# Kernel optimization log

Hardware: AMD Instinct MI355X
Metric: run time of the kernel (lower is better)

The kernel has to match this reference:

```python
import jax, jax.numpy as jnp
import numpy as np

B, CIN, COUT, K, H, W = 8, 256, 256, 3, 64, 64
STRIDE, PAD, DIL, DG = 1, 1, 1, 1
K2 = K * K


def _conv2d(x, w, b):
    out = jax.lax.conv_general_dilated(
        x, w, (STRIDE, STRIDE), [(PAD, PAD), (PAD, PAD)],
        rhs_dilation=(DIL, DIL),
        dimension_numbers=('NCHW', 'OIHW', 'NCHW'))
    return out + b[None, :, None, None]


def _deform_conv2d(x, offset, mask, weight, bias):
    # torchvision.ops.deform_conv2d semantics (DCNv2, bilinear, zero outside).
    Bn, Cin, Hin, Win = x.shape
    O = weight.shape[0]
    dg, Cg = DG, Cin // DG
    Ho, Wo = offset.shape[2], offset.shape[3]
    # offset channel layout: [dg, K2, (dy,dx)] interleaved per kernel point
    off = offset.reshape(Bn, dg, K2, 2, Ho, Wo)
    dy, dx = off[:, :, :, 0], off[:, :, :, 1]
    m = mask.reshape(Bn, dg, K2, Ho, Wo)
    ky, kx = jnp.meshgrid(jnp.arange(K), jnp.arange(K), indexing='ij')
    ky = ky.reshape(K2).astype(x.dtype)
    kx = kx.reshape(K2).astype(x.dtype)
    base_y = jnp.arange(Ho, dtype=x.dtype) * STRIDE - PAD
    base_x = jnp.arange(Wo, dtype=x.dtype) * STRIDE - PAD
    # sampling positions [B, dg, K2, Ho, Wo]
    py = base_y[None, None, None, :, None] + (ky * DIL)[None, None, :, None, None] + dy
    px = base_x[None, None, None, None, :] + (kx * DIL)[None, None, :, None, None] + dx
    y0 = jnp.floor(py)
    x0 = jnp.floor(px)
    ly, lx = py - y0, px - x0

    xflat = x.reshape(Bn, dg, Cg, Hin * Win)

    def gather_one(xg, idx):
        return jnp.take(xg, idx, axis=1)

    gather = jax.vmap(jax.vmap(gather_one))  # over B, dg

    def corner(yc, xc, wgt):
        valid = (yc >= 0) & (yc <= Hin - 1) & (xc >= 0) & (xc <= Win - 1)
        yi = jnp.clip(yc, 0, Hin - 1).astype(jnp.int32)
        xi = jnp.clip(xc, 0, Win - 1).astype(jnp.int32)
        idx = (yi * Win + xi).reshape(Bn, dg, K2 * Ho * Wo)
        v = gather(xflat, idx).reshape(Bn, dg, Cg, K2, Ho, Wo)
        w = jnp.where(valid, wgt, jnp.zeros_like(wgt))
        return v * w[:, :, None]  # broadcast over Cg

    sampled = (corner(y0, x0, (1 - ly) * (1 - lx))
               + corner(y0, x0 + 1, (1 - ly) * lx)
               + corner(y0 + 1, x0, ly * (1 - lx))
               + corner(y0 + 1, x0 + 1, ly * lx))
    sampled = sampled * m[:, :, None]  # modulation mask
    wk = weight.reshape(O, dg, Cg, K2)
    out = jnp.einsum('ogck,bgckhw->bohw', wk, sampled)
    return out + bias[None, :, None, None]


def reference(x, weight, bias, w_off, b_off):
    om = _conv2d(x, w_off, b_off)  # [B, 3*dg*K2, H, W]
    n = DG * K2
    o1, o2, mask = om[:, :n], om[:, n:2 * n], om[:, 2 * n:]
    offset = jnp.concatenate([o1, o2], axis=1)
    mask = jax.nn.sigmoid(mask)
    return _deform_conv2d(x, offset, mask, weight, bias)


def setup_inputs():
    key = jax.random.key(0)
    k1, k2, k3, k4, k5 = jax.random.split(key, 5)
    fan_in = CIN * K2
    bound = 1.0 / np.sqrt(fan_in).astype(np.float32)
    x = jax.random.normal(k1, (B, CIN, H, W), dtype=jnp.float32)
    weight = jax.random.uniform(k2, (COUT, CIN, K, K), minval=-bound, maxval=bound, dtype=jnp.float32)
    bias = jax.random.uniform(k3, (COUT,), minval=-bound, maxval=bound, dtype=jnp.float32)
    # small random offset-conv params (zero init in the source is degenerate)
    w_off = jax.random.normal(k4, (3 * K2 * DG, CIN, K, K), dtype=jnp.float32) * 0.01
    b_off = jax.random.normal(k5, (3 * K2 * DG,), dtype=jnp.float32) * 0.01
    return {"x": x, "weight": weight, "bias": bias, "w_off": w_off, "b_off": b_off}
```

## Files before the change

### kernel.cpp

```cpp
#include <hip/hip_runtime.h>
#include <hip/hip_bf16.h>
#include <stdint.h>

typedef short bf16x8 __attribute__((ext_vector_type(8)));
typedef float f32x4  __attribute__((ext_vector_type(4)));

#define NB   8
#define NC   256
#define NO   256
#define HH   64
#define WW   64
#define NPIX 4096
#define KTOT 2304
#define NKC  72

#define XN_OFF  0u
#define XN_SZ   (NB*NPIX*NC*2u)
#define WP_OFF  (XN_OFF + XN_SZ)
#define WP_SZ   (KTOT*NO*2u)
#define WPO_OFF (WP_OFF + WP_SZ)
#define WPO_SZ  (KTOT*32u*2u)
#define OM_OFF  (WPO_OFF + WPO_SZ)
#define OM_SZ   (NB*NPIX*32u*4u)
#define PY_OFF  (OM_OFF + OM_SZ)
#define CO_SZ   (NB*9u*NPIX*4u)
#define PX_OFF  (PY_OFF + CO_SZ)
#define MK_OFF  (PX_OFF + CO_SZ)

__device__ __forceinline__ float b2f(short s) {
    union { unsigned u; float f; } z; z.u = ((unsigned)(unsigned short)s) << 16; return z.f;
}
__device__ __forceinline__ short f2b(float f) {
    __hip_bfloat16 h = __float2bfloat16(f);
    short s; __builtin_memcpy(&s, &h, 2); return s;
}

__global__ void pack_x(const float* __restrict__ x, unsigned short* __restrict__ xn) {
    __shared__ float tile[64][65];
    int blk = blockIdx.x;
    int pt = blk & 63, ct = (blk >> 6) & 3, b = blk >> 8;
    int t = threadIdx.x;
    int pi = t & 63, ci0 = t >> 6;
    const float* src = x + ((size_t)(b*NC + ct*64))*NPIX + (size_t)pt*64;
#pragma unroll
    for (int j = 0; j < 16; ++j)
        tile[ci0 + 4*j][pi] = src[(size_t)(ci0 + 4*j)*NPIX + pi];
    __syncthreads();
    int c = t & 63, pj0 = t >> 6;
    unsigned short* dst = xn + ((size_t)b*NPIX + (size_t)pt*64)*NC + ct*64;
#pragma unroll
    for (int j = 0; j < 16; ++j) {
        int pj = pj0 + 4*j;
        dst[(size_t)pj*NC + c] = (unsigned short)f2b(tile[c][pj]);
    }
}

__global__ void pack_w(const float* __restrict__ weight, unsigned short* __restrict__ wp) {
    int idx = blockIdx.x*256 + threadIdx.x;
    int e = idx & 7, l = (idx >> 3) & 63, nt = (idx >> 9) & 15, kc = idx >> 13;
    int k  = kc*32 + 8*(l >> 4) + e;
    int k2 = k >> 8, c = k & 255;
    int ky = k2 / 3, kx = k2 - 3*ky;
    int o  = nt*16 + (l & 15);
    float v = weight[(size_t)(o*NC + c)*9 + ky*3 + kx];
    wp[idx] = (unsigned short)f2b(v);
}

__global__ void pack_wo(const float* __restrict__ w_off, unsigned short* __restrict__ wpo) {
    int idx = blockIdx.x*256 + threadIdx.x;
    int e = idx & 7, l = (idx >> 3) & 63, nt = (idx >> 9) & 1, kc = idx >> 10;
    int k  = kc*32 + 8*(l >> 4) + e;
    int k2 = k >> 8, c = k & 255;
    int ky = k2 / 3, kx = k2 - 3*ky;
    int n  = nt*16 + (l & 15);
    float v = (n < 27) ? w_off[(size_t)(n*NC + c)*9 + ky*3 + kx] : 0.0f;
    wpo[idx] = (unsigned short)f2b(v);
}

__launch_bounds__(256, 2)
__global__ void off_conv(const unsigned short* __restrict__ xn,
                         const unsigned short* __restrict__ wpo,
                         float* __restrict__ om) {
    int blk = blockIdx.x;
    int mt = blk & 63, b = blk >> 6;
    int t = threadIdx.x, wv = t >> 6, l = t & 63, g = l >> 4;
    int pix = mt*64 + wv*16 + (l & 15);
    int y = pix >> 6, xx = pix & 63;
    f32x4 acc0 = {0.f,0.f,0.f,0.f}, acc1 = {0.f,0.f,0.f,0.f};
    const unsigned short* xb = xn + (size_t)b*NPIX*NC;
    const bf16x8* wpf = (const bf16x8*)wpo;
    for (int kc = 0; kc < NKC; ++kc) {
        int k2 = kc >> 3, cc = kc & 7;
        int ky = k2 / 3, kx = k2 - 3*ky;
        int sy = y + ky - 1, sx = xx + kx - 1;
        bool valid = (sy >= 0) & (sy < HH) & (sx >= 0) & (sx < WW);
        bf16x8 a = {0,0,0,0,0,0,0,0};
        if (valid)
            a = *(const bf16x8*)(xb + (size_t)(sy*WW + sx)*NC + cc*32 + g*8);
        bf16x8 b0 = wpf[(size_t)(kc*2    )*64 + l];
        bf16x8 b1 = wpf[(size_t)(kc*2 + 1)*64 + l];
        acc0 = __builtin_amdgcn_mfma_f32_16x16x32_bf16(a, b0, acc0, 0, 0, 0);
        acc1 = __builtin_amdgcn_mfma_f32_16x16x32_bf16(a, b1, acc1, 0, 0, 0);
    }
#pragma unroll
    for (int r = 0; r < 4; ++r) {
        int pm = mt*64 + wv*16 + 4*g + r;
        om[((size_t)b*NPIX + pm)*32 +      (l & 15)] = acc0[r];
        om[((size_t)b*NPIX + pm)*32 + 16 + (l & 15)] = acc1[r];
    }
}

__global__ void coords_k(const float* __restrict__ om, const float* __restrict__ b_off,
                         float* __restrict__ py, float* __restrict__ px,
                         float* __restrict__ mk) {
    int idx = blockIdx.x*256 + threadIdx.x;
    if (idx >= NB*9*NPIX) return;
    int pix = idx & 4095;
    int k   = (idx >> 12) % 9;
    int b   = idx / (9*NPIX);
    const float* omp = om + ((size_t)b*NPIX + pix)*32;
    float dy = omp[2*k]     + b_off[2*k];
    float dx = omp[2*k + 1] + b_off[2*k + 1];
    float m  = omp[18 + k]  + b_off[18 + k];
    float yy = (float)(pix >> 6) - 1.0f + (float)(k / 3) + dy;
    float xv = (float)(pix & 63) - 1.0f + (float)(k % 3) + dx;
    py[idx] = yy;
    px[idx] = xv;
    mk[idx] = 1.0f / (1.0f + __expf(-m));
}

__launch_bounds__(256, 2)
__global__ void dcn_main(const unsigned short* __restrict__ xn,
                         const unsigned short* __restrict__ wpack,
                         const float* __restrict__ pyA,
                         const float* __restrict__ pxA,
                         const float* __restrict__ mkA,
                         const float* __restrict__ bias,
                         float* __restrict__ out) {
    __shared__ unsigned short lds[2][8192];
    int blk = blockIdx.x;
    int mt = blk & 63, b = blk >> 6;
    int t = threadIdx.x, wv = t >> 6, l = t & 63, g = l >> 4;
    int pixm = mt*64 + wv*16 + (l & 15);

    f32x4 acc[16];
#pragma unroll
    for (int i = 0; i < 16; ++i) acc[i] = f32x4{0.f,0.f,0.f,0.f};

    const unsigned short* xb = xn + (size_t)b*NPIX*NC;

#define STAGE(bi, kcs) do {                                                            \
        const unsigned short* _gs = wpack + (size_t)(kcs)*8192 + wv*2048 + l*8;        \
        _Pragma("unroll")                                                              \
        for (int _i = 0; _i < 4; ++_i) {                                               \
            __builtin_amdgcn_global_load_lds(                                          \
                (const __attribute__((address_space(1))) unsigned int*)(_gs + _i*512), \
                (__attribute__((address_space(3))) unsigned int*)(&lds[bi][wv*2048 + _i*512]), \
                16, 0, 0);                                                             \
        }                                                                              \
    } while (0)

    float cw0 = 0.f, cw1 = 0.f, cw2 = 0.f, cw3 = 0.f;
    unsigned ca0 = 0, ca1 = 0, ca2 = 0, ca3 = 0;

    STAGE(0, 0);
    __syncthreads();
    int buf = 0;
    for (int kc = 0; kc < NKC; ++kc) {
        int k2 = kc >> 3, cc = kc & 7;
        if (cc == 0) {
            int ci = ((b*9 + k2) << 12) + pixm;
            float py = pyA[ci], px = pxA[ci], m = mkA[ci];
            float y0f = floorf(py), x0f = floorf(px);
            float ly = py - y0f, lx = px - x0f;
            int iy0 = (int)y0f, ix0 = (int)x0f;
            int iy1 = iy0 + 1,  ix1 = ix0 + 1;
            bool vy0 = (iy0 >= 0) & (iy0 < HH);
            bool vy1 = (iy1 >= 0) & (iy1 < HH);
            bool vx0 = (ix0 >= 0) & (ix0 < WW);
            bool vx1 = (ix1 >= 0) & (ix1 < WW);
            float wy0 = (1.f - ly) * m, wy1 = ly * m;
            cw0 = (vy0 & vx0) ? wy0 * (1.f - lx) : 0.f;
            cw1 = (vy0 & vx1) ? wy0 * lx         : 0.f;
            cw2 = (vy1 & vx0) ? wy1 * (1.f - lx) : 0.f;
            cw3 = (vy1 & vx1) ? wy1 * lx         : 0.f;
            int cy0 = min(max(iy0, 0), HH-1), cy1 = min(max(iy1, 0), HH-1);
            int cx0 = min(max(ix0, 0), WW-1), cx1 = min(max(ix1, 0), WW-1);
            ca0 = (unsigned)(((cy0*WW + cx0)*NC + g*8) * 2);
            ca1 = (unsigned)(((cy0*WW + cx1)*NC + g*8) * 2);
            ca2 = (unsigned)(((cy1*WW + cx0)*NC + g*8) * 2);
            ca3 = (unsigned)(((cy1*WW + cx1)*NC + g*8) * 2);
        }
        if (kc < NKC-1) STAGE(buf ^ 1, kc + 1);

        unsigned co = (unsigned)cc * 64u;
        const char* xc = (const char*)xb;
        bf16x8 v00 = *(const bf16x8*)(xc + ca0 + co);
        bf16x8 v01 = *(const bf16x8*)(xc + ca1 + co);
        bf16x8 v10 = *(const bf16x8*)(xc + ca2 + co);
        bf16x8 v11 = *(const bf16x8*)(xc + ca3 + co);
        bf16x8 a;
#pragma unroll
        for (int e = 0; e < 8; ++e) {
            float f = cw0*b2f(v00[e]) + cw1*b2f(v01[e]) + cw2*b2f(v10[e]) + cw3*b2f(v11[e]);
            a[e] = f2b(f);
        }
        const bf16x8* bl = (const bf16x8*)&lds[buf][0];
#pragma unroll
        for (int nt = 0; nt < 16; ++nt)
            acc[nt] = __builtin_amdgcn_mfma_f32_16x16x32_bf16(a, bl[nt*64 + l], acc[nt], 0, 0, 0);
        __syncthreads();
        buf ^= 1;
    }
#undef STAGE

    int pm = mt*64 + wv*16 + 4*g;
#pragma unroll
    for (int nt = 0; nt < 16; ++nt) {
        int o = nt*16 + (l & 15);
        float bv = bias[o];
        f32x4 r = acc[nt] + bv;
        *(f32x4*)(out + ((size_t)(b*NO + o))*NPIX + pm) = r;
    }
}

extern "C" void kernel_launch(void* const* d_in, const int* in_sizes, int n_in,
                              void* d_out, int out_size, void* d_ws, size_t ws_size,
                              hipStream_t stream) {
    const float* x      = (const float*)d_in[0];
    const float* weight = (const float*)d_in[1];
    const float* bias   = (const float*)d_in[2];
    const float* w_off  = (const float*)d_in[3];
    const float* b_off  = (const float*)d_in[4];
    float* out = (float*)d_out;
    char* ws = (char*)d_ws;

    unsigned short* xn  = (unsigned short*)(ws + XN_OFF);
    unsigned short* wp  = (unsigned short*)(ws + WP_OFF);
    unsigned short* wpo = (unsigned short*)(ws + WPO_OFF);
    float* om = (float*)(ws + OM_OFF);
    float* py = (float*)(ws + PY_OFF);
    float* px = (float*)(ws + PX_OFF);
    float* mk = (float*)(ws + MK_OFF);

    pack_x  <<<2048, 256, 0, stream>>>(x, xn);
    pack_w  <<<KTOT*NO/256,  256, 0, stream>>>(weight, wp);
    pack_wo <<<KTOT*32/256,  256, 0, stream>>>(w_off, wpo);
    off_conv<<<512, 256, 0, stream>>>(xn, wpo, om);
    coords_k<<<NB*9*NPIX/256, 256, 0, stream>>>(om, b_off, py, px, mk);
    dcn_main<<<512, 256, 0, stream>>>(xn, wp, py, px, mk, bias, out);
}
```

Before: 221.5 us.

## Retile deform-conv main kernel to 128 pixels x 128 outputs with software-pipelined gathers

Result: slower. 265.5 us (+19.8%).

```diff
diff --git a/kernel.cpp b/kernel.cpp
--- a/kernel.cpp
+++ b/kernel.cpp
@@ -81,26 +81,45 @@
 __global__ void off_conv(const unsigned short* __restrict__ xn,
                          const unsigned short* __restrict__ wpo,
                          float* __restrict__ om) {
-    int blk = blockIdx.x;
-    int mt = blk & 63, b = blk >> 6;
+    int bid = blockIdx.x;
+    int lid = (bid & 7)*64 + (bid >> 3);
+    int mt = lid & 63, b = lid >> 6;
     int t = threadIdx.x, wv = t >> 6, l = t & 63, g = l >> 4;
     int pix = mt*64 + wv*16 + (l & 15);
     int y = pix >> 6, xx = pix & 63;
     f32x4 acc0 = {0.f,0.f,0.f,0.f}, acc1 = {0.f,0.f,0.f,0.f};
-    const unsigned short* xb = xn + (size_t)b*NPIX*NC;
+    const char* xc = (const char*)(xn + (size_t)b*NPIX*NC);
     const bf16x8* wpf = (const bf16x8*)wpo;
-    for (int kc = 0; kc < NKC; ++kc) {
+    const bf16x8 zero8 = {0,0,0,0,0,0,0,0};
+
+    auto aaddr = [&](int kc)->const char* {
         int k2 = kc >> 3, cc = kc & 7;
         int ky = k2 / 3, kx = k2 - 3*ky;
         int sy = y + ky - 1, sx = xx + kx - 1;
-        bool valid = (sy >= 0) & (sy < HH) & (sx >= 0) & (sx < WW);
-        bf16x8 a = {0,0,0,0,0,0,0,0};
-        if (valid)
-            a = *(const bf16x8*)(xb + (size_t)(sy*WW + sx)*NC + cc*32 + g*8);
-        bf16x8 b0 = wpf[(size_t)(kc*2    )*64 + l];
-        bf16x8 b1 = wpf[(size_t)(kc*2 + 1)*64 + l];
-        acc0 = __builtin_amdgcn_mfma_f32_16x16x32_bf16(a, b0, acc0, 0, 0, 0);
-        acc1 = __builtin_amdgcn_mfma_f32_16x16x32_bf16(a, b1, acc1, 0, 0, 0);
+        int cs = min(max(sy,0),HH-1)*WW + min(max(sx,0),WW-1);
+        return xc + ((size_t)cs*NC + cc*32 + g*8)*2;
+    };
+    auto avalid = [&](int kc)->bool {
+        int k2 = kc >> 3;
+        int ky = k2 / 3, kx = k2 - 3*ky;
+        int sy = y + ky - 1, sx = xx + kx - 1;
+        return (sy>=0)&(sy<HH)&(sx>=0)&(sx<WW);
+    };
+
+    bf16x8 a_c = *(const bf16x8*)aaddr(0);
+    bf16x8 w0c = wpf[l], w1c = wpf[64 + l];
+    bool v_c = avalid(0);
+#pragma unroll
+    for (int kc = 0; kc < NKC; ++kc) {
+        int kn = (kc < NKC-1) ? kc+1 : kc;
+        bf16x8 a_n = *(const bf16x8*)aaddr(kn);
+        bf16x8 w0n = wpf[(size_t)(kn*2)*64 + l];
+        bf16x8 w1n = wpf[(size_t)(kn*2+1)*64 + l];
+        bool v_n = avalid(kn);
+        bf16x8 au = v_c ? a_c : zero8;
+        acc0 = __builtin_amdgcn_mfma_f32_16x16x32_bf16(au, w0c, acc0, 0, 0, 0);
+        acc1 = __builtin_amdgcn_mfma_f32_16x16x32_bf16(au, w1c, acc1, 0, 0, 0);
+        a_c = a_n; w0c = w0n; w1c = w1n; v_c = v_n;
     }
 #pragma unroll
     for (int r = 0; r < 4; ++r) {
@@ -137,91 +156,141 @@
                          const float* __restrict__ mkA,
                          const float* __restrict__ bias,
                          float* __restrict__ out) {
-    __shared__ unsigned short lds[2][8192];
-    int blk = blockIdx.x;
-    int mt = blk & 63, b = blk >> 6;
+    __shared__ unsigned short lds[2][4096];
+    int bid = blockIdx.x;
+    int lid = (bid & 7)*64 + (bid >> 3);
+    int nh  = lid & 1;
+    int mtg = lid >> 1;
+    int mt = mtg & 31, b = mtg >> 5;
     int t = threadIdx.x, wv = t >> 6, l = t & 63, g = l >> 4;
-    int pixm = mt*64 + wv*16 + (l & 15);
-
-    f32x4 acc[16];
-#pragma unroll
-    for (int i = 0; i < 16; ++i) acc[i] = f32x4{0.f,0.f,0.f,0.f};
-
-    const unsigned short* xb = xn + (size_t)b*NPIX*NC;
-
-#define STAGE(bi, kcs) do {                                                            \
-        const unsigned short* _gs = wpack + (size_t)(kcs)*8192 + wv*2048 + l*8;        \
+    int pix0 = mt*128 + wv*32 + (l & 15);
+
+    f32x4 acc[2][8];
+#pragma unroll
+    for (int f = 0; f < 2; ++f)
+#pragma unroll
+        for (int nt = 0; nt < 8; ++nt) acc[f][nt] = f32x4{0.f,0.f,0.f,0.f};
+
+    const char* xc = (const char*)(xn + (size_t)b*NPIX*NC);
+    const unsigned short* wpb = wpack + nh*4096 + wv*1024 + l*8;
+
+    float cw[2][4];  const char* bp[2][4];
+    float ncw[2][4]; const char* nbp[2][4];
+    float npy[2], npx[2], nm[2];
+
+    auto coord_compute = [&](float py, float px, float m, float* cwf, const char** bpf) {
+        float y0f = floorf(py), x0f = floorf(px);
+        float ly = py - y0f, lx = px - x0f;
+        int iy0 = (int)y0f, ix0 = (int)x0f;
+        int iy1 = iy0 + 1,  ix1 = ix0 + 1;
+        bool vy0 = (iy0 >= 0) & (iy0 < HH);
+        bool vy1 = (iy1 >= 0) & (iy1 < HH);
+        bool vx0 = (ix0 >= 0) & (ix0 < WW);
+        bool vx1 = (ix1 >= 0) & (ix1 < WW);
+        float wy0 = (1.f - ly) * m, wy1 = ly * m;
+        cwf[0] = (vy0 & vx0) ? wy0 * (1.f - lx) : 0.f;
+        cwf[1] = (vy0 & vx1) ? wy0 * lx         : 0.f;
+        cwf[2] = (vy1 & vx0) ? wy1 * (1.f - lx) : 0.f;
+        cwf[3] = (vy1 & vx1) ? wy1 * lx         : 0.f;
+        int cy0 = min(max(iy0,0),HH-1), cy1 = min(max(iy1,0),HH-1);
+        int cx0 = min(max(ix0,0),WW-1), cx1 = min(max(ix1,0),WW-1);
+        bpf[0] = xc + ((size_t)(cy0*WW + cx0)*NC + g*8)*2;
+        bpf[1] = xc + ((size_t)(cy0*WW + cx1)*NC + g*8)*2;
+        bpf[2] = xc + ((size_t)(cy1*WW + cx0)*NC + g*8)*2;
+        bpf[3] = xc + ((size_t)(cy1*WW + cx1)*NC + g*8)*2;
+    };
+
+#define STAGEW(bi, kcs) do {                                                           \
+        const unsigned short* _gs = wpb + (size_t)(kcs)*8192;                          \
         _Pragma("unroll")                                                              \
-        for (int _i = 0; _i < 4; ++_i) {                                               \
+        for (int _i = 0; _i < 2; ++_i) {                                               \
             __builtin_amdgcn_global_load_lds(                                          \
                 (const __attribute__((address_space(1))) unsigned int*)(_gs + _i*512), \
-                (__attribute__((address_space(3))) unsigned int*)(&lds[bi][wv*2048 + _i*512]), \
+                (__attribute__((address_space(3))) unsigned int*)(&lds[bi][wv*1024 + _i*512]), \
                 16, 0, 0);                                                             \
         }                                                                              \
     } while (0)
 
-    float cw0 = 0.f, cw1 = 0.f, cw2 = 0.f, cw3 = 0.f;
-    unsigned ca0 = 0, ca1 = 0, ca2 = 0, ca3 = 0;
-
-    STAGE(0, 0);
+#pragma unroll
+    for (int f = 0; f < 2; ++f) {
+        int ci = ((b*9) << 12) + pix0 + f*16;
+        coord_compute(pyA[ci], pxA[ci], mkA[ci], cw[f], bp[f]);
+    }
+    bf16x8 cur[2][4], nxt[2][4];
+#pragma unroll
+    for (int f = 0; f < 2; ++f)
+#pragma unroll
+        for (int c = 0; c < 4; ++c)
+            cur[f][c] = *(const bf16x8*)bp[f][c];
+    STAGEW(0, 0);
     __syncthreads();
-    int buf = 0;
-    for (int kc = 0; kc < NKC; ++kc) {
-        int k2 = kc >> 3, cc = kc & 7;
-        if (cc == 0) {
-            int ci = ((b*9 + k2) << 12) + pixm;
-            float py = pyA[ci], px = pxA[ci], m = mkA[ci];
-            float y0f = floorf(py), x0f = floorf(px);
-            float ly = py - y0f, lx = px - x0f;
-            int iy0 = (int)y0f, ix0 = (int)x0f;
-            int iy1 = iy0 + 1,  ix1 = ix0 + 1;
-            bool vy0 = (iy0 >= 0) & (iy0 < HH);
-            bool vy1 = (iy1 >= 0) & (iy1 < HH);
-            bool vx0 = (ix0 >= 0) & (ix0 < WW);
-            bool vx1 = (ix1 >= 0) & (ix1 < WW);
-            float wy0 = (1.f - ly) * m, wy1 = ly * m;
-            cw0 = (vy0 & vx0) ? wy0 * (1.f - lx) : 0.f;
-            cw1 = (vy0 & vx1) ? wy0 * lx         : 0.f;
-            cw2 = (vy1 & vx0) ? wy1 * (1.f - lx) : 0.f;
-            cw3 = (vy1 & vx1) ? wy1 * lx         : 0.f;
-            int cy0 = min(max(iy0, 0), HH-1), cy1 = min(max(iy1, 0), HH-1);
-            int cx0 = min(max(ix0, 0), WW-1), cx1 = min(max(ix1, 0), WW-1);
-            ca0 = (unsigned)(((cy0*WW + cx0)*NC + g*8) * 2);
-            ca1 = (unsigned)(((cy0*WW + cx1)*NC + g*8) * 2);
-            ca2 = (unsigned)(((cy1*WW + cx0)*NC + g*8) * 2);
-            ca3 = (unsigned)(((cy1*WW + cx1)*NC + g*8) * 2);
+
+    for (int k2 = 0; k2 < 9; ++k2) {
+        int k2n = (k2 < 8) ? k2 + 1 : 8;
+#pragma unroll
+        for (int cc = 0; cc < 8; ++cc) {
+            int kc = k2*8 + cc;
+            if (kc < NKC-1) STAGEW((kc+1) & 1, kc+1);
+            if (cc == 2) {
+#pragma unroll
+                for (int f = 0; f < 2; ++f) {
+                    int ci = ((b*9 + k2n) << 12) + pix0 + f*16;
+                    npy[f] = pyA[ci]; npx[f] = pxA[ci]; nm[f] = mkA[ci];
+                }
+            }
+            if (cc == 5) {
+#pragma unroll
+                for (int f = 0; f < 2; ++f)
+                    coord_compute(npy[f], npx[f], nm[f], ncw[f], nbp[f]);
+            }
+#pragma unroll
+            for (int f = 0; f < 2; ++f)
+#pragma unroll
+                for (int c = 0; c < 4; ++c)
+                    nxt[f][c] = (cc < 7) ? *(const bf16x8*)(bp[f][c] + (cc+1)*64)
+                                         : *(const bf16x8*)(nbp[f][c]);
+            bf16x8 af[2];
+#pragma unroll
+            for (int f = 0; f < 2; ++f) {
+#pragma unroll
+                for (int e = 0; e < 8; ++e) {
+                    float v = cw[f][0]*b2f(cur[f][0][e]) + cw[f][1]*b2f(cur[f][1][e])
+                            + cw[f][2]*b2f(cur[f][2][e]) + cw[f][3]*b2f(cur[f][3][e]);
+                    af[f][e] = f2b(v);
+                }
+            }
+            const bf16x8* bl = (const bf16x8*)&lds[kc & 1][0];
+#pragma unroll
+            for (int nt = 0; nt < 8; ++nt) {
+                bf16x8 wf = bl[nt*64 + l];
+                acc[0][nt] = __builtin_amdgcn_mfma_f32_16x16x32_bf16(af[0], wf, acc[0][nt], 0, 0, 0);
+                acc[1][nt] = __builtin_amdgcn_mfma_f32_16x16x32_bf16(af[1], wf, acc[1][nt], 0, 0, 0);
+            }
+            __syncthreads();
+#pragma unroll
+            for (int f = 0; f < 2; ++f)
+#pragma unroll
+                for (int c = 0; c < 4; ++c)
+                    cur[f][c] = nxt[f][c];
+            if (cc == 7) {
+#pragma unroll
+                for (int f = 0; f < 2; ++f)
+#pragma unroll
+                    for (int c = 0; c < 4; ++c) { cw[f][c] = ncw[f][c]; bp[f][c] = nbp[f][c]; }
+            }
         }
-        if (kc < NKC-1) STAGE(buf ^ 1, kc + 1);
-
-        unsigned co = (unsigned)cc * 64u;
-        const char* xc = (const char*)xb;
-        bf16x8 v00 = *(const bf16x8*)(xc + ca0 + co);
-        bf16x8 v01 = *(const bf16x8*)(xc + ca1 + co);
-        bf16x8 v10 = *(const bf16x8*)(xc + ca2 + co);
-        bf16x8 v11 = *(const bf16x8*)(xc + ca3 + co);
-        bf16x8 a;
-#pragma unroll
-        for (int e = 0; e < 8; ++e) {
-            float f = cw0*b2f(v00[e]) + cw1*b2f(v01[e]) + cw2*b2f(v10[e]) + cw3*b2f(v11[e]);
-            a[e] = f2b(f);
+    }
+#undef STAGEW
+
+#pragma unroll
+    for (int f = 0; f < 2; ++f)
+#pragma unroll
+        for (int nt = 0; nt < 8; ++nt) {
+            int o = nh*128 + nt*16 + (l & 15);
+            float bv = bias[o];
+            f32x4 r = acc[f][nt] + bv;
+            *(f32x4*)(out + ((size_t)(b*NO + o))*NPIX + (mt*128 + wv*32 + f*16 + 4*g)) = r;
         }
-        const bf16x8* bl = (const bf16x8*)&lds[buf][0];
-#pragma unroll
-        for (int nt = 0; nt < 16; ++nt)
-            acc[nt] = __builtin_amdgcn_mfma_f32_16x16x32_bf16(a, bl[nt*64 + l], acc[nt], 0, 0, 0);
-        __syncthreads();
-        buf ^= 1;
-    }
-#undef STAGE
-
-    int pm = mt*64 + wv*16 + 4*g;
-#pragma unroll
-    for (int nt = 0; nt < 16; ++nt) {
-        int o = nt*16 + (l & 15);
-        float bv = bias[o];
-        f32x4 r = acc[nt] + bv;
-        *(f32x4*)(out + ((size_t)(b*NO + o))*NPIX + pm) = r;
-    }
 }
 
 extern "C" void kernel_launch(void* const* d_in, const int* in_sizes, int n_in,
```

## Split deformable conv into explicit im2col sampling and tiled MFMA GEMM

Applied to the files above, without the earlier changes.

New measurement: 250.9 us. 13.3% more time.

```diff
diff --git a/kernel.cpp b/kernel.cpp
--- a/kernel.cpp
+++ b/kernel.cpp
@@ -4,6 +4,7 @@
 
 typedef short bf16x8 __attribute__((ext_vector_type(8)));
 typedef float f32x4  __attribute__((ext_vector_type(4)));
+typedef int   i32x4  __attribute__((ext_vector_type(4)));
 
 #define NB   8
 #define NC   256
@@ -13,6 +14,7 @@
 #define NPIX 4096
 #define KTOT 2304
 #define NKC  72
+#define NMF  2048
 
 #define XN_OFF  0u
 #define XN_SZ   (NB*NPIX*NC*2u)
@@ -26,6 +28,8 @@
 #define CO_SZ   (NB*9u*NPIX*4u)
 #define PX_OFF  (PY_OFF + CO_SZ)
 #define MK_OFF  (PX_OFF + CO_SZ)
+#define AM_OFF  (MK_OFF + CO_SZ)
+#define AM_SZ   ((size_t)NKC*NMF*1024ull)
 
 __device__ __forceinline__ float b2f(short s) {
     union { unsigned u; float f; } z; z.u = ((unsigned)(unsigned short)s) << 16; return z.f;
@@ -33,6 +37,27 @@
 __device__ __forceinline__ short f2b(float f) {
     __hip_bfloat16 h = __float2bfloat16(f);
     short s; __builtin_memcpy(&s, &h, 2); return s;
+}
+__device__ __forceinline__ float dw_lo(int u) {
+    union { int i; float f; } z; z.i = u << 16; return z.f;
+}
+__device__ __forceinline__ float dw_hi(int u) {
+    union { int i; float f; } z; z.i = u & 0xFFFF0000; return z.f;
+}
+
+__device__ __forceinline__ bf16x8 blend4(bf16x8 c0, bf16x8 c1, bf16x8 c2, bf16x8 c3,
+                                         float w0, float w1, float w2, float w3) {
+    union U { bf16x8 s; i32x4 i; } u0, u1, u2, u3, r;
+    u0.s = c0; u1.s = c1; u2.s = c2; u3.s = c3;
+#pragma unroll
+    for (int d = 0; d < 4; ++d) {
+        float lo = w0*dw_lo(u0.i[d]) + w1*dw_lo(u1.i[d]) + w2*dw_lo(u2.i[d]) + w3*dw_lo(u3.i[d]);
+        float hi = w0*dw_hi(u0.i[d]) + w1*dw_hi(u1.i[d]) + w2*dw_hi(u2.i[d]) + w3*dw_hi(u3.i[d]);
+        int pk;
+        asm("v_cvt_pk_bf16_f32 %0, %1, %2" : "=v"(pk) : "v"(lo), "v"(hi));
+        r.i[d] = pk;
+    }
+    return r.s;
 }
 
 __global__ void pack_x(const float* __restrict__ x, unsigned short* __restrict__ xn) {
@@ -40,18 +65,26 @@
     int blk = blockIdx.x;
     int pt = blk & 63, ct = (blk >> 6) & 3, b = blk >> 8;
     int t = threadIdx.x;
-    int pi = t & 63, ci0 = t >> 6;
+    int ci = t >> 4, p4 = (t & 15) * 4;
     const float* src = x + ((size_t)(b*NC + ct*64))*NPIX + (size_t)pt*64;
 #pragma unroll
-    for (int j = 0; j < 16; ++j)
-        tile[ci0 + 4*j][pi] = src[(size_t)(ci0 + 4*j)*NPIX + pi];
+    for (int j = 0; j < 4; ++j) {
+        f32x4 v = *(const f32x4*)(src + (size_t)(ci + 16*j)*NPIX + p4);
+        tile[ci + 16*j][p4+0] = v[0];
+        tile[ci + 16*j][p4+1] = v[1];
+        tile[ci + 16*j][p4+2] = v[2];
+        tile[ci + 16*j][p4+3] = v[3];
+    }
     __syncthreads();
-    int c = t & 63, pj0 = t >> 6;
-    unsigned short* dst = xn + ((size_t)b*NPIX + (size_t)pt*64)*NC + ct*64;
-#pragma unroll
-    for (int j = 0; j < 16; ++j) {
-        int pj = pj0 + 4*j;
-        dst[(size_t)pj*NC + c] = (unsigned short)f2b(tile[c][pj]);
+    int c8 = (t & 7) * 8, pj0 = t >> 3;
+    unsigned short* dst = xn + ((size_t)b*NPIX + (size_t)pt*64)*NC + ct*64 + c8;
+#pragma unroll
+    for (int j = 0; j < 2; ++j) {
+        int pj = pj0 + 32*j;
+        bf16x8 o;
+#pragma unroll
+        for (int e = 0; e < 8; ++e) o[e] = f2b(tile[c8 + e][pj]);
+        *(bf16x8*)(dst + (size_t)pj*NC) = o;
     }
 }
 
@@ -77,36 +110,36 @@
     wpo[idx] = (unsigned short)f2b(v);
 }
 
-__launch_bounds__(256, 2)
+__launch_bounds__(256, 4)
 __global__ void off_conv(const unsigned short* __restrict__ xn,
                          const unsigned short* __restrict__ wpo,
                          float* __restrict__ om) {
-    int blk = blockIdx.x;
-    int mt = blk & 63, b = blk >> 6;
-    int t = threadIdx.x, wv = t >> 6, l = t & 63, g = l >> 4;
-    int pix = mt*64 + wv*16 + (l & 15);
+    int bid = blockIdx.x;
+    int b = bid & 7, rr = bid >> 3;
+    int t = threadIdx.x, wv = t >> 6, l = t & 63, g = l >> 4, l15 = l & 15;
+    int wid = rr*4 + wv;
+    int mt = wid >> 1, nh = wid & 1;
+    int pix = mt*16 + l15;
     int y = pix >> 6, xx = pix & 63;
-    f32x4 acc0 = {0.f,0.f,0.f,0.f}, acc1 = {0.f,0.f,0.f,0.f};
-    const unsigned short* xb = xn + (size_t)b*NPIX*NC;
+    f32x4 acc = {0.f,0.f,0.f,0.f};
+    const char* xc = (const char*)(xn + (size_t)b*NPIX*NC);
     const bf16x8* wpf = (const bf16x8*)wpo;
+    const bf16x8 zero8 = {0,0,0,0,0,0,0,0};
+#pragma unroll
     for (int kc = 0; kc < NKC; ++kc) {
         int k2 = kc >> 3, cc = kc & 7;
         int ky = k2 / 3, kx = k2 - 3*ky;
         int sy = y + ky - 1, sx = xx + kx - 1;
-        bool valid = (sy >= 0) & (sy < HH) & (sx >= 0) & (sx < WW);
-        bf16x8 a = {0,0,0,0,0,0,0,0};
-        if (valid)
-            a = *(const bf16x8*)(xb + (size_t)(sy*WW + sx)*NC + cc*32 + g*8);
-        bf16x8 b0 = wpf[(size_t)(kc*2    )*64 + l];
-        bf16x8 b1 = wpf[(size_t)(kc*2 + 1)*64 + l];
-        acc0 = __builtin_amdgcn_mfma_f32_16x16x32_bf16(a, b0, acc0, 0, 0, 0);
-        acc1 = __builtin_amdgcn_mfma_f32_16x16x32_bf16(a, b1, acc1, 0, 0, 0);
+        bool valid = (sy>=0)&(sy<HH)&(sx>=0)&(sx<WW);
+        int cs = min(max(sy,0),HH-1)*WW + min(max(sx,0),WW-1);
+        bf16x8 a = *(const bf16x8*)(xc + ((size_t)cs*NC + cc*32 + g*8)*2);
+        bf16x8 w = wpf[(size_t)(kc*2 + nh)*64 + l];
+        acc = __builtin_amdgcn_mfma_f32_16x16x32_bf16(valid ? a : zero8, w, acc, 0, 0, 0);
     }
 #pragma unroll
     for (int r = 0; r < 4; ++r) {
-        int pm = mt*64 + wv*16 + 4*g + r;
-        om[((size_t)b*NPIX + pm)*32 +      (l & 15)] = acc0[r];
-        om[((size_t)b*NPIX + pm)*32 + 16 + (l & 15)] = acc1[r];
+        int pm = mt*16 + 4*g + r;
+        om[((size_t)b*NPIX + pm)*32 + nh*16 + l15] = acc[r];
     }
 }
 
@@ -129,14 +162,131 @@
     mk[idx] = 1.0f / (1.0f + __expf(-m));
 }
 
-__launch_bounds__(256, 2)
-__global__ void dcn_main(const unsigned short* __restrict__ xn,
-                         const unsigned short* __restrict__ wpack,
+__launch_bounds__(256, 4)
+__global__ void sample_a(const unsigned short* __restrict__ xn,
                          const float* __restrict__ pyA,
                          const float* __restrict__ pxA,
                          const float* __restrict__ mkA,
-                         const float* __restrict__ bias,
-                         float* __restrict__ out) {
+                         unsigned short* __restrict__ am) {
+    int bid = blockIdx.x;
+    int lid = (bid & 7)*576 + (bid >> 3);
+    int t = threadIdx.x, wv = t >> 6, l = t & 63, g = l >> 4, l15 = l & 15;
+    int wg = lid*4 + wv;
+    int mf = wg / 9, k2 = wg - 9*mf;
+    int pixg = mf*16 + l15;
+    int b = pixg >> 12, pix = pixg & 4095;
+    const char* xc = (const char*)(xn + (size_t)b*NPIX*NC);
+    int ci = ((b*9 + k2) << 12) + pix;
+    float py = pyA[ci], px = pxA[ci], m = mkA[ci];
+
+    float y0f = floorf(py), x0f = floorf(px);
+    float ly = py - y0f, lx = px - x0f;
+    int iy0 = (int)y0f, ix0 = (int)x0f;
+    int iy1 = iy0 + 1,  ix1 = ix0 + 1;
+    bool vy0 = (iy0 >= 0) & (iy0 < HH);
+    bool vy1 = (iy1 >= 0) & (iy1 < HH);
+    bool vx0 = (ix0 >= 0) & (ix0 < WW);
+    bool vx1 = (ix1 >= 0) & (ix1 < WW);
+    float wy0 = (1.f - ly) * m, wy1 = ly * m;
+    float cw0 = (vy0 & vx0) ? wy0 * (1.f - lx) : 0.f;
+    float cw1 = (vy0 & vx1) ? wy0 * lx         : 0.f;
+    float cw2 = (vy1 & vx0) ? wy1 * (1.f - lx) : 0.f;
+    float cw3 = (vy1 & vx1) ? wy1 * lx         : 0.f;
+    int cy0 = min(max(iy0,0),HH-1), cy1 = min(max(iy1,0),HH-1);
+    int cx0 = min(max(ix0,0),WW-1), cx1 = min(max(ix1,0),WW-1);
+    unsigned co0 = (unsigned)(((cy0*WW + cx0)*NC + g*8) * 2);
+    unsigned co1 = (unsigned)(((cy0*WW + cx1)*NC + g*8) * 2);
+    unsigned co2 = (unsigned)(((cy1*WW + cx0)*NC + g*8) * 2);
+    unsigned co3 = (unsigned)(((cy1*WW + cx1)*NC + g*8) * 2);
+
+    unsigned short* dst = am + ((size_t)(k2*8)*NMF + mf)*512 + l*8;
+#pragma unroll
+    for (int cc = 0; cc < 8; ++cc) {
+        unsigned cb = (unsigned)cc * 64u;
+        bf16x8 c0 = *(const bf16x8*)(xc + co0 + cb);
+        bf16x8 c1 = *(const bf16x8*)(xc + co1 + cb);
+        bf16x8 c2 = *(const bf16x8*)(xc + co2 + cb);
+        bf16x8 c3 = *(const bf16x8*)(xc + co3 + cb);
+        bf16x8 af = blend4(c0, c1, c2, c3, cw0, cw1, cw2, cw3);
+        *(bf16x8*)(dst + (size_t)cc*NMF*512) = af;
+    }
+}
+
+__launch_bounds__(256, 2)
+__global__ void gemm_a(const unsigned short* __restrict__ am,
+                       const unsigned short* __restrict__ wpack,
+                       const float* __restrict__ bias,
+                       float* __restrict__ out) {
+    __shared__ unsigned short lds[2][8192];
+    int bid = blockIdx.x;
+    int lid = (bid & 7)*64 + (bid >> 3);
+    int mt = lid >> 1, nh = lid & 1;
+    int t = threadIdx.x, l = t & 63, g = l >> 4, l15 = l & 15;
+    int wv = t >> 6, wm = wv >> 1, wn = wv & 1;
+
+    f32x4 acc[4][4];
+#pragma unroll
+    for (int i = 0; i < 4; ++i)
+#pragma unroll
+        for (int j = 0; j < 4; ++j) acc[i][j] = f32x4{0.f,0.f,0.f,0.f};
+
+#define GLDS(gp, lp)                                                        \
+    __builtin_amdgcn_global_load_lds(                                       \
+        (const __attribute__((address_space(1))) unsigned int*)(gp),        \
+        (__attribute__((address_space(3))) unsigned int*)(lp), 16, 0, 0)
+
+    auto stage = [&](int buf, int kc) {
+        const unsigned short* ga = am    + ((size_t)kc*NMF + mt*8)*512 + t*8;
+        const unsigned short* gb = wpack + ((size_t)kc*16 + nh*8)*512 + t*8;
+        unsigned short* la = &lds[buf][0]    + t*8;
+        unsigned short* lb = &lds[buf][4096] + t*8;
+        GLDS(ga,        la);
+        GLDS(ga + 2048, la + 2048);
+        GLDS(gb,        lb);
+        GLDS(gb + 2048, lb + 2048);
+    };
+
+    stage(0, 0);
+    __syncthreads();
+    for (int kc = 0; kc < NKC; ++kc) {
+        int buf = kc & 1;
+        if (kc < NKC-1) stage(buf ^ 1, kc + 1);
+        const bf16x8* A  = (const bf16x8*)&lds[buf][0];
+        const bf16x8* Bf = (const bf16x8*)&lds[buf][4096];
+        bf16x8 a[4], bq[4];
+#pragma unroll
+        for (int i = 0; i < 4; ++i) a[i]  = A [(wm*4 + i)*64 + l];
+#pragma unroll
+        for (int j = 0; j < 4; ++j) bq[j] = Bf[(wn*4 + j)*64 + l];
+#pragma unroll
+        for (int i = 0; i < 4; ++i)
+#pragma unroll
+            for (int j = 0; j < 4; ++j)
+                acc[i][j] = __builtin_amdgcn_mfma_f32_16x16x32_bf16(a[i], bq[j], acc[i][j], 0, 0, 0);
+        __syncthreads();
+    }
+#undef GLDS
+
+    int b  = mt >> 5;
+    int pb = (mt & 31)*128 + wm*64 + 4*g;
+#pragma unroll
+    for (int i = 0; i < 4; ++i)
+#pragma unroll
+        for (int j = 0; j < 4; ++j) {
+            int o = nh*128 + wn*64 + j*16 + l15;
+            f32x4 r = acc[i][j] + bias[o];
+            *(f32x4*)(out + ((size_t)(b*NO + o))*NPIX + pb + i*16) = r;
+        }
+}
+
+__launch_bounds__(256, 2)
+__global__ void dcn_fused(const unsigned short* __restrict__ xn,
+                          const unsigned short* __restrict__ wpack,
+                          const float* __restrict__ pyA,
+                          const float* __restrict__ pxA,
+                          const float* __restrict__ mkA,
+                          const float* __restrict__ bias,
+                          float* __restrict__ out) {
     __shared__ unsigned short lds[2][8192];
     int blk = blockIdx.x;
     int mt = blk & 63, b = blk >> 6;
@@ -194,17 +344,12 @@
         if (kc < NKC-1) STAGE(buf ^ 1, kc + 1);
 
         unsigned co = (unsigned)cc * 64u;
-        const char* xc = (const char*)xb;
-        bf16x8 v00 = *(const bf16x8*)(xc + ca0 + co);
-        bf16x8 v01 = *(const bf16x8*)(xc + ca1 + co);
-        bf16x8 v10 = *(const bf16x8*)(xc + ca2 + co);
-        bf16x8 v11 = *(const bf16x8*)(xc + ca3 + co);
-        bf16x8 a;
-#pragma unroll
-        for (int e = 0; e < 8; ++e) {
-            float f = cw0*b2f(v00[e]) + cw1*b2f(v01[e]) + cw2*b2f(v10[e]) + cw3*b2f(v11[e]);
-            a[e] = f2b(f);
-        }
+        const char* xcc = (const char*)xb;
+        bf16x8 v00 = *(const bf16x8*)(xcc + ca0 + co);
+        bf16x8 v01 = *(const bf16x8*)(xcc + ca1 + co);
+        bf16x8 v10 = *(const bf16x8*)(xcc + ca2 + co);
+        bf16x8 v11 = *(const bf16x8*)(xcc + ca3 + co);
+        bf16x8 a = blend4(v00, v01, v10, v11, cw0, cw1, cw2, cw3);
         const bf16x8* bl = (const bf16x8*)&lds[buf][0];
 #pragma unroll
         for (int nt = 0; nt < 16; ++nt)
@@ -242,11 +387,18 @@
     float* py = (float*)(ws + PY_OFF);
     float* px = (float*)(ws + PX_OFF);
     float* mk = (float*)(ws + MK_OFF);
+    unsigned short* am  = (unsigned short*)(ws + AM_OFF);
 
     pack_x  <<<2048, 256, 0, stream>>>(x, xn);
     pack_w  <<<KTOT*NO/256,  256, 0, stream>>>(weight, wp);
     pack_wo <<<KTOT*32/256,  256, 0, stream>>>(w_off, wpo);
-    off_conv<<<512, 256, 0, stream>>>(xn, wpo, om);
+    off_conv<<<1024, 256, 0, stream>>>(xn, wpo, om);
     coords_k<<<NB*9*NPIX/256, 256, 0, stream>>>(om, b_off, py, px, mk);
-    dcn_main<<<512, 256, 0, stream>>>(xn, wp, py, px, mk, bias, out);
-}
+
+    if (ws_size >= (size_t)AM_OFF + AM_SZ) {
+        sample_a<<<4608, 256, 0, stream>>>(xn, py, px, mk, am);
+        gemm_a  <<<512,  256, 0, stream>>>(am, wp, bias, out);
+    } else {
+        dcn_fused<<<512, 256, 0, stream>>>(xn, wp, py, px, mk, bias, out);
+    }
+}
```
